# Optimization experiments

Hardware: AMD Instinct MI355X
Metric: run time of the kernel (lower is better)

Reference implementation:

```python
import jax, jax.numpy as jnp
import numpy as np

EPS = 1e-5

@jax.custom_vjp
def ste_sign(x):
    # Binarize: sign(x); backward is straight-through identity (BNN convention)
    return jnp.sign(x)

def _ste_fwd(x):
    return jnp.sign(x), None

def _ste_bwd(_, g):
    return (g,)

ste_sign.defvjp(_ste_fwd, _ste_bwd)

def bn(y, gamma, beta, mean, var):
    # inference-mode BatchNorm2d over channel axis 1
    inv = gamma * jax.lax.rsqrt(var + EPS)
    return y * inv[None, :, None, None] + (beta - mean * inv)[None, :, None, None]

def setup_inputs() -> dict:
    key = jax.random.key(0)
    ks = jax.random.split(key, 11)
    B, C, H, W = 32, 256, 56, 56
    return {
        "x":  jax.random.normal(ks[0], (B, C, H, W), jnp.float32),
        "w1": jax.random.normal(ks[1], (3 * C, C), jnp.float32),   # 1x1 conv kernel [out,in]
        "w2": jax.random.normal(ks[2], (C, 3 * C), jnp.float32),
        "g1": jax.random.uniform(ks[3], (3 * C,), jnp.float32, 0.5, 1.5),
        "b1": jax.random.normal(ks[4], (3 * C,), jnp.float32),
        "m1": jax.random.normal(ks[5], (3 * C,), jnp.float32),
        "v1": jax.random.uniform(ks[6], (3 * C,), jnp.float32, 0.5, 1.5),
        "g2": jax.random.uniform(ks[7], (C,), jnp.float32, 0.5, 1.5),
        "b2": jax.random.normal(ks[8], (C,), jnp.float32),
        "m2": jax.random.normal(ks[9], (C,), jnp.float32),
        "v2": jax.random.uniform(ks[10], (C,), jnp.float32, 0.5, 1.5),
    }

def reference(x, w1, w2, g1, b1, m1, v1, g2, b2, m2, v2):
    # BinarizeConv2d: binarize input + weight, 1x1 conv == channel GEMM
    y1 = jnp.einsum('oc,bchw->bohw', ste_sign(w1), ste_sign(x))
    y1 = bn(y1, g1, b1, m1, v1)
    y2 = jnp.einsum('oc,bchw->bohw', ste_sign(w2), ste_sign(y1))
    y2 = bn(y2, g2, b2, m2, v2)
    return y2 + x
```

## Files before the change

kernel.cpp:

```cpp
#include <hip/hip_runtime.h>

typedef unsigned long long u64;

#define HW    3136
#define CIN   256
#define CMID  768
#define EPSV  1e-5

__global__ __launch_bounds__(64) void prep_kernel(
    const float* __restrict__ w1, const float* __restrict__ w2,
    const float* __restrict__ g1, const float* __restrict__ b1,
    const float* __restrict__ m1, const float* __restrict__ v1,
    const float* __restrict__ g2, const float* __restrict__ b2,
    const float* __restrict__ m2, const float* __restrict__ v2,
    u64* __restrict__ pw1, u64* __restrict__ pw2,
    int* __restrict__ t1, float2* __restrict__ ab2)
{
  int blk  = blockIdx.x;
  int lane = threadIdx.x;
  if (blk < 3072) {
    int o = blk >> 2, seg = blk & 3;
    u64 msk = __ballot(w1[o * CIN + (seg << 6) + lane] < 0.0f);
    if (lane == 0) pw1[blk] = msk;
  } else if (blk < 6144) {
    int i = blk - 3072;
    int o = i / 12, seg = i - o * 12;
    u64 msk = __ballot(w2[o * CMID + (seg << 6) + lane] < 0.0f);
    if (lane == 0) pw2[i] = msk;
  } else {
    int i = ((blk - 6144) << 6) + lane;
    if (i < CMID) {
      double inv = (double)g1[i] / sqrt((double)v1[i] + EPSV);
      double c   = (double)b1[i] - (double)m1[i] * inv;
      t1[i] = (int)floor(256.0 + c / inv);
    } else if (i < CMID + CIN) {
      int j = i - CMID;
      double inv = (double)g2[j] / sqrt((double)v2[j] + EPSV);
      float2 o2;
      o2.x = (float)(-2.0 * inv);
      o2.y = (float)(768.0 * inv + (double)b2[j] - (double)m2[j] * inv);
      ab2[j] = o2;
    }
  }
}

__global__ __launch_bounds__(256, 6) void bnn_kernel(
    const float* __restrict__ x,
    const u64* __restrict__ pw1, const u64* __restrict__ pw2,
    const int* __restrict__ t1g, const float2* __restrict__ ab2g,
    float* __restrict__ out)
{
  __shared__ u64 ssx[4][64];
  __shared__ u64 szx[4][64];
  __shared__ u64 ssy[64][13];
  __shared__ u64 szf[4];

  int t    = threadIdx.x;
  int w    = t >> 6;
  int lane = t & 63;
  int px0  = blockIdx.x * 64;

  u64 w1r[3][4]; int t1r[3];
  #pragma unroll
  for (int k = 0; k < 3; ++k) {
    int o = w * 192 + (k << 6) + lane;
    ulonglong2 a  = *(const ulonglong2*)&pw1[(size_t)(o << 2)];
    ulonglong2 bq = *(const ulonglong2*)&pw1[(size_t)(o << 2) + 2];
    w1r[k][0] = a.x; w1r[k][1] = a.y; w1r[k][2] = bq.x; w1r[k][3] = bq.y;
    t1r[k] = t1g[o];
  }

  {
    int px = px0 + lane;
    int pb = px / HW, phw = px - pb * HW;
    const float* xp = x + (size_t)pb * (CIN * HW) + phw + (size_t)(w << 6) * HW;
    u64 s = 0, z = 0;
    #pragma unroll 8
    for (int c = 0; c < 64; ++c) {
      unsigned u = __float_as_uint(xp[(size_t)c * HW]);
      s |= (u64)(u >> 31) << c;
      z |= (u64)((u + u) == 0u ? 1u : 0u) << c;
    }
    ssx[w][lane] = s;
    szx[w][lane] = z;
    u64 zb = __ballot(z != 0ull);
    if (lane == 0) szf[w] = zb;
  }
  __syncthreads();

  u64 zm = szf[0] | szf[1] | szf[2] | szf[3];

  u64 c0 = 0, c1 = 0, c2 = 0;
  #pragma unroll 4
  for (int q = 0; q < 64; ++q) {
    u64 x0 = ssx[0][q], x1 = ssx[1][q], x2 = ssx[2][q], x3 = ssx[3][q];
    int pv0, pv1, pv2;
    {
      int pk;
      pk = __popcll(w1r[0][0] ^ x0) + __popcll(w1r[0][1] ^ x1)
         + __popcll(w1r[0][2] ^ x2) + __popcll(w1r[0][3] ^ x3);
      pv0 = pk + pk;
      pk = __popcll(w1r[1][0] ^ x0) + __popcll(w1r[1][1] ^ x1)
         + __popcll(w1r[1][2] ^ x2) + __popcll(w1r[1][3] ^ x3);
      pv1 = pk + pk;
      pk = __popcll(w1r[2][0] ^ x0) + __popcll(w1r[2][1] ^ x1)
         + __popcll(w1r[2][2] ^ x2) + __popcll(w1r[2][3] ^ x3);
      pv2 = pk + pk;
    }
    if (__builtin_expect((int)((zm >> q) & 1ull), 0)) {
      u64 z0 = szx[0][q], z1 = szx[1][q], z2 = szx[2][q], z3 = szx[3][q];
      int K0 = __popcll(z0) + __popcll(z1) + __popcll(z2) + __popcll(z3);
      #pragma unroll
      for (int k = 0; k < 3; ++k) {
        int dz = __popcll((w1r[k][0] ^ x0) & z0)
               + __popcll((w1r[k][1] ^ x1) & z1)
               + __popcll((w1r[k][2] ^ x2) & z2)
               + __popcll((w1r[k][3] ^ x3) & z3);
        int adj = K0 - dz - dz;
        if (k == 0) pv0 += adj; else if (k == 1) pv1 += adj; else pv2 += adj;
      }
    }
    u64 b0 = __ballot(pv0 > t1r[0]);
    u64 b1 = __ballot(pv1 > t1r[1]);
    u64 b2 = __ballot(pv2 > t1r[2]);
    if (lane == q) { c0 = b0; c1 = b1; c2 = b2; }
  }

  ssy[lane][3 * w + 0] = c0;
  ssy[lane][3 * w + 1] = c1;
  ssy[lane][3 * w + 2] = c2;
  __syncthreads();

  u64 sy[12];
  #pragma unroll
  for (int j = 0; j < 12; ++j) sy[j] = ssy[lane][j];

  int px = px0 + lane;
  int pb = px / HW, phw = px - pb * HW;
  const float* xr = x   + (size_t)pb * (CIN * HW) + phw;
  float*       op = out + (size_t)pb * (CIN * HW) + phw;

  int ob = w << 6;
  #pragma unroll 2
  for (int j = 0; j < 64; ++j) {
    int o  = ob + j;
    int ou = __builtin_amdgcn_readfirstlane(o);
    const u64* wr = pw2 + (size_t)ou * 12;
    float2 ab = ab2g[ou];
    int pa = __popcll(wr[0] ^ sy[0])  + __popcll(wr[1]  ^ sy[1])
           + __popcll(wr[2] ^ sy[2])  + __popcll(wr[3]  ^ sy[3])
           + __popcll(wr[4] ^ sy[4])  + __popcll(wr[5]  ^ sy[5]);
    int pb2 = __popcll(wr[6] ^ sy[6])  + __popcll(wr[7]  ^ sy[7])
            + __popcll(wr[8] ^ sy[8])  + __popcll(wr[9]  ^ sy[9])
            + __popcll(wr[10] ^ sy[10]) + __popcll(wr[11] ^ sy[11]);
    float y = fmaf((float)(pa + pb2), ab.x, ab.y);
    op[(size_t)o * HW] = y + xr[(size_t)o * HW];
  }
}

extern "C" void kernel_launch(void* const* d_in, const int* in_sizes, int n_in,
                              void* d_out, int out_size, void* d_ws, size_t ws_size,
                              hipStream_t stream) {
  const float* x  = (const float*)d_in[0];
  const float* w1 = (const float*)d_in[1];
  const float* w2 = (const float*)d_in[2];
  const float* g1 = (const float*)d_in[3];
  const float* b1 = (const float*)d_in[4];
  const float* m1 = (const float*)d_in[5];
  const float* v1 = (const float*)d_in[6];
  const float* g2 = (const float*)d_in[7];
  const float* b2 = (const float*)d_in[8];
  const float* m2 = (const float*)d_in[9];
  const float* v2 = (const float*)d_in[10];
  float* out = (float*)d_out;

  u64*    pw1 = (u64*)d_ws;
  u64*    pw2 = pw1 + 3072;
  int*    t1  = (int*)(pw2 + 3072);
  float2* ab2 = (float2*)(t1 + CMID);

  prep_kernel<<<6160, 64, 0, stream>>>(w1, w2, g1, b1, m1, v1,
                                       g2, b2, m2, v2, pw1, pw2, t1, ab2);
  bnn_kernel<<<1568, 256, 0, stream>>>(x, pw1, pw2, t1, ab2, out);
}
```

Before: 127.1 us.

## Prefetch residual loads in groups, transpose sign-bit LDS layout, lazily compute zero masks

The epilogue now loads the residual x values in double-buffered groups of 16 registers ahead of the popcount/store work, so global load latency overlaps compute. The shared sign and zero bitmasks are transposed to [pixel][word] so each q iteration reads them with two 128-bit LDS loads, with the next row prefetched. The zero-mask build is replaced by a running min that only triggers a second pass over x when an exact zero is present. The cost is higher register pressure from 32 float buffers and prefetched vectors, which may limit occupancy under the 6-wave launch bound.

```diff
diff --git a/kernel.cpp b/kernel.cpp
--- a/kernel.cpp
+++ b/kernel.cpp
@@ -50,8 +50,8 @@
     const int* __restrict__ t1g, const float2* __restrict__ ab2g,
     float* __restrict__ out)
 {
-  __shared__ u64 ssx[4][64];
-  __shared__ u64 szx[4][64];
+  __shared__ __align__(16) u64 ssx[64][6];
+  __shared__ __align__(16) u64 szx[64][6];
   __shared__ u64 ssy[64][13];
   __shared__ u64 szf[4];
 
@@ -74,15 +74,24 @@
     int px = px0 + lane;
     int pb = px / HW, phw = px - pb * HW;
     const float* xp = x + (size_t)pb * (CIN * HW) + phw + (size_t)(w << 6) * HW;
-    u64 s = 0, z = 0;
+    u64 s = 0;
+    unsigned mn = ~0u;
     #pragma unroll 8
     for (int c = 0; c < 64; ++c) {
       unsigned u = __float_as_uint(xp[(size_t)c * HW]);
       s |= (u64)(u >> 31) << c;
-      z |= (u64)((u + u) == 0u ? 1u : 0u) << c;
-    }
-    ssx[w][lane] = s;
-    szx[w][lane] = z;
+      unsigned m = u + u;
+      mn = mn < m ? mn : m;
+    }
+    ssx[lane][w] = s;
+    u64 z = 0;
+    if (__builtin_expect(mn == 0u, 0)) {
+      for (int c = 0; c < 64; ++c) {
+        unsigned u = __float_as_uint(xp[(size_t)c * HW]);
+        z |= (u64)((u + u) == 0u ? 1u : 0u) << c;
+      }
+    }
+    szx[lane][w] = z;
     u64 zb = __ballot(z != 0ull);
     if (lane == 0) szf[w] = zb;
   }
@@ -91,31 +100,38 @@
   u64 zm = szf[0] | szf[1] | szf[2] | szf[3];
 
   u64 c0 = 0, c1 = 0, c2 = 0;
+  ulonglong2 xaN = *(const ulonglong2*)&ssx[0][0];
+  ulonglong2 xbN = *(const ulonglong2*)&ssx[0][2];
   #pragma unroll 4
   for (int q = 0; q < 64; ++q) {
-    u64 x0 = ssx[0][q], x1 = ssx[1][q], x2 = ssx[2][q], x3 = ssx[3][q];
+    ulonglong2 xa = xaN, xb = xbN;
+    if (q < 63) {
+      xaN = *(const ulonglong2*)&ssx[q + 1][0];
+      xbN = *(const ulonglong2*)&ssx[q + 1][2];
+    }
     int pv0, pv1, pv2;
     {
       int pk;
-      pk = __popcll(w1r[0][0] ^ x0) + __popcll(w1r[0][1] ^ x1)
-         + __popcll(w1r[0][2] ^ x2) + __popcll(w1r[0][3] ^ x3);
+      pk = __popcll(w1r[0][0] ^ xa.x) + __popcll(w1r[0][1] ^ xa.y)
+         + __popcll(w1r[0][2] ^ xb.x) + __popcll(w1r[0][3] ^ xb.y);
       pv0 = pk + pk;
-      pk = __popcll(w1r[1][0] ^ x0) + __popcll(w1r[1][1] ^ x1)
-         + __popcll(w1r[1][2] ^ x2) + __popcll(w1r[1][3] ^ x3);
+      pk = __popcll(w1r[1][0] ^ xa.x) + __popcll(w1r[1][1] ^ xa.y)
+         + __popcll(w1r[1][2] ^ xb.x) + __popcll(w1r[1][3] ^ xb.y);
       pv1 = pk + pk;
-      pk = __popcll(w1r[2][0] ^ x0) + __popcll(w1r[2][1] ^ x1)
-         + __popcll(w1r[2][2] ^ x2) + __popcll(w1r[2][3] ^ x3);
+      pk = __popcll(w1r[2][0] ^ xa.x) + __popcll(w1r[2][1] ^ xa.y)
+         + __popcll(w1r[2][2] ^ xb.x) + __popcll(w1r[2][3] ^ xb.y);
       pv2 = pk + pk;
     }
     if (__builtin_expect((int)((zm >> q) & 1ull), 0)) {
-      u64 z0 = szx[0][q], z1 = szx[1][q], z2 = szx[2][q], z3 = szx[3][q];
-      int K0 = __popcll(z0) + __popcll(z1) + __popcll(z2) + __popcll(z3);
+      ulonglong2 za = *(const ulonglong2*)&szx[q][0];
+      ulonglong2 zb = *(const ulonglong2*)&szx[q][2];
+      int K0 = __popcll(za.x) + __popcll(za.y) + __popcll(zb.x) + __popcll(zb.y);
       #pragma unroll
       for (int k = 0; k < 3; ++k) {
-        int dz = __popcll((w1r[k][0] ^ x0) & z0)
-               + __popcll((w1r[k][1] ^ x1) & z1)
-               + __popcll((w1r[k][2] ^ x2) & z2)
-               + __popcll((w1r[k][3] ^ x3) & z3);
+        int dz = __popcll((w1r[k][0] ^ xa.x) & za.x)
+               + __popcll((w1r[k][1] ^ xa.y) & za.y)
+               + __popcll((w1r[k][2] ^ xb.x) & zb.x)
+               + __popcll((w1r[k][3] ^ xb.y) & zb.y);
         int adj = K0 - dz - dz;
         if (k == 0) pv0 += adj; else if (k == 1) pv1 += adj; else pv2 += adj;
       }
@@ -139,23 +155,39 @@
   int pb = px / HW, phw = px - pb * HW;
   const float* xr = x   + (size_t)pb * (CIN * HW) + phw;
   float*       op = out + (size_t)pb * (CIN * HW) + phw;
-
   int ob = w << 6;
-  #pragma unroll 2
-  for (int j = 0; j < 64; ++j) {
-    int o  = ob + j;
-    int ou = __builtin_amdgcn_readfirstlane(o);
-    const u64* wr = pw2 + (size_t)ou * 12;
-    float2 ab = ab2g[ou];
-    int pa = __popcll(wr[0] ^ sy[0])  + __popcll(wr[1]  ^ sy[1])
-           + __popcll(wr[2] ^ sy[2])  + __popcll(wr[3]  ^ sy[3])
-           + __popcll(wr[4] ^ sy[4])  + __popcll(wr[5]  ^ sy[5]);
-    int pb2 = __popcll(wr[6] ^ sy[6])  + __popcll(wr[7]  ^ sy[7])
-            + __popcll(wr[8] ^ sy[8])  + __popcll(wr[9]  ^ sy[9])
-            + __popcll(wr[10] ^ sy[10]) + __popcll(wr[11] ^ sy[11]);
-    float y = fmaf((float)(pa + pb2), ab.x, ab.y);
-    op[(size_t)o * HW] = y + xr[(size_t)o * HW];
-  }
+
+#define LOADG(RX, G)                                                          \
+  _Pragma("unroll") for (int i = 0; i < 16; ++i)                              \
+    RX[i] = xr[(size_t)(ob + (G) * 16 + i) * HW];
+
+#define COMPG(RX, G)                                                          \
+  _Pragma("unroll") for (int j = 0; j < 16; ++j) {                            \
+    int o  = ob + (G) * 16 + j;                                               \
+    int ou = __builtin_amdgcn_readfirstlane(o);                               \
+    const u64* wr = pw2 + (size_t)ou * 12;                                    \
+    float2 ab = ab2g[ou];                                                     \
+    int pa = __popcll(wr[0] ^ sy[0])  + __popcll(wr[1]  ^ sy[1])              \
+           + __popcll(wr[2] ^ sy[2])  + __popcll(wr[3]  ^ sy[3])              \
+           + __popcll(wr[4] ^ sy[4])  + __popcll(wr[5]  ^ sy[5]);             \
+    int pb2 = __popcll(wr[6] ^ sy[6])  + __popcll(wr[7]  ^ sy[7])             \
+            + __popcll(wr[8] ^ sy[8])  + __popcll(wr[9]  ^ sy[9])             \
+            + __popcll(wr[10] ^ sy[10]) + __popcll(wr[11] ^ sy[11]);          \
+    float y = fmaf((float)(pa + pb2), ab.x, ab.y);                            \
+    op[(size_t)o * HW] = y + RX[j];                                           \
+  }
+
+  float rxA[16], rxB[16];
+  LOADG(rxA, 0);
+  LOADG(rxB, 1);
+  COMPG(rxA, 0);
+  LOADG(rxA, 2);
+  COMPG(rxB, 1);
+  LOADG(rxB, 3);
+  COMPG(rxA, 2);
+  COMPG(rxB, 3);
+#undef LOADG
+#undef COMPG
 }
 
 extern "C" void kernel_launch(void* const* d_in, const int* in_sizes, int n_in,
```

Result: slower. 134.6 us (+5.9%).
